# Kernel optimization log

Measured on AMD Instinct MI355X. Metric: run time of the kernel, lower is better.

Reference implementation:

```python
import jax, jax.numpy as jnp
import numpy as np

H = 1024  # hidden_dim
M = 4     # num_modalities
B = 8192  # batch


def setup_inputs() -> dict:
    key = jax.random.key(0)
    ks = jax.random.split(key, 10)
    s = 1.0 / np.sqrt(H)  # torch Linear default init scale
    return {
        "features": jax.random.normal(ks[0], (B, M, H), dtype=jnp.float32),
        "confidences": jax.random.uniform(ks[1], (B, M, 1), dtype=jnp.float32),
        "Wq": jax.random.uniform(ks[2], (H, H), jnp.float32, -s, s),
        "bq": jax.random.uniform(ks[3], (H,), jnp.float32, -s, s),
        "Wk": jax.random.uniform(ks[4], (H, H), jnp.float32, -s, s),
        "bk": jax.random.uniform(ks[5], (H,), jnp.float32, -s, s),
        "Wv": jax.random.uniform(ks[6], (H, H), jnp.float32, -s, s),
        "bv": jax.random.uniform(ks[7], (H,), jnp.float32, -s, s),
        "Wo": jax.random.uniform(ks[8], (H, H), jnp.float32, -s, s),
        "bo": jax.random.uniform(ks[9], (H,), jnp.float32, -s, s),
    }


def reference(features, confidences, Wq, bq, Wk, bk, Wv, bv, Wo, bo):
    # features: [B, M, H], confidences: [B, M, 1]
    q = jnp.einsum('bmh,oh->bmo', features, Wq) + bq
    k = jnp.einsum('bmh,oh->bmo', features, Wk) + bk
    v = jnp.einsum('bmh,oh->bmo', features, Wv) + bv
    scores = jnp.einsum('bmh,bnh->bmn', q, k) / jnp.sqrt(jnp.float32(features.shape[-1]))
    scores = scores * confidences  # [B,M,1] broadcasts over last (key) axis
    attn = jax.nn.softmax(scores, axis=-1)           # [B, M, M]
    attended = jnp.einsum('bmn,bnh->bmh', attn, v)   # [B, M, H]
    fused = jnp.mean(attended, axis=1)               # [B, H]
    return fused @ Wo.T + bo
```

## Files before the change

### kernel.cpp

```cpp
#include <hip/hip_runtime.h>


typedef unsigned short u16;
typedef unsigned char u8;
typedef __attribute__((ext_vector_type(8))) __bf16 bf16x8;
typedef __attribute__((ext_vector_type(4))) float floatx4;
typedef __attribute__((ext_vector_type(16))) float floatx16;
typedef __attribute__((ext_vector_type(8))) int intx8;

__device__ __forceinline__ u16 f2bf(float f) {
    unsigned u = __float_as_uint(f);
    unsigned r = (u + 0x7FFFu + ((u >> 16) & 1u)) >> 16;
    return (u16)r;
}

__device__ __forceinline__ unsigned f2e4m3(float x) {
    unsigned u = __float_as_uint(x);
    unsigned s = (u >> 31) << 7;
    float a = __uint_as_float(u & 0x7FFFFFFFu);
    if (a >= 448.f) return s | 0x7E;
    if (a < 0.03125f) {
        unsigned k = (unsigned)__float2int_rn(a * 512.f);
        return s | k;
    }
    unsigned b = __float_as_uint(a);
    unsigned lsb = (b >> 20) & 1u;
    b += 0x0007FFFFu + lsb;
    unsigned ex = (b >> 23) - 120u;
    unsigned man = (b >> 20) & 7u;
    return s | (ex << 3) | man;
}

__device__ __forceinline__ void load_lds16(const void* g, void* l) {
    __builtin_amdgcn_global_load_lds(
        (const __attribute__((address_space(1))) void*)g,
        (__attribute__((address_space(3))) void*)l, 16, 0, 0);
}

__device__ __forceinline__ void unpack8(uint4 v, float* f) {
    f[0] = __uint_as_float(v.x << 16);
    f[1] = __uint_as_float(v.x & 0xFFFF0000u);
    f[2] = __uint_as_float(v.y << 16);
    f[3] = __uint_as_float(v.y & 0xFFFF0000u);
    f[4] = __uint_as_float(v.z << 16);
    f[5] = __uint_as_float(v.z & 0xFFFF0000u);
    f[6] = __uint_as_float(v.w << 16);
    f[7] = __uint_as_float(v.w & 0xFFFF0000u);
}

__global__ __launch_bounds__(256) void k_cast(const float* __restrict__ in,
                                              u16* __restrict__ outb,
                                              u8* __restrict__ outf, long n) {
    long i = ((long)blockIdx.x * 256 + threadIdx.x) * 4;
    if (i < n) {
        float4 v = *(const float4*)(in + i);
        ushort4 o;
        o.x = f2bf(v.x); o.y = f2bf(v.y); o.z = f2bf(v.z); o.w = f2bf(v.w);
        *(ushort4*)(outb + i) = o;
        if (outf) {
            unsigned p = f2e4m3(v.x) | (f2e4m3(v.y) << 8) |
                         (f2e4m3(v.z) << 16) | (f2e4m3(v.w) << 24);
            *(unsigned*)(outf + i) = p;
        }
    }
}

__global__ __launch_bounds__(256) void k_prep(const float* __restrict__ Wq,
                                              const float* __restrict__ Wk,
                                              const float* __restrict__ Wv,
                                              const float* __restrict__ Wo,
                                              u16* __restrict__ WqT,
                                              u16* __restrict__ WkT,
                                              u16* __restrict__ WvT,
                                              u16* __restrict__ Wob, int H) {
    __shared__ float t[32][33];
    const int z = blockIdx.z;
    const float* in = (z == 0) ? Wk : (z == 1) ? Wq : (z == 2) ? Wv : Wo;
    u16* out = (z == 0) ? WkT : (z == 1) ? WqT : (z == 2) ? WvT : Wob;
    int bx = blockIdx.x * 32, by = blockIdx.y * 32;
    int x = threadIdx.x;
    if (z < 3) {
        for (int y = threadIdx.y; y < 32; y += 8)
            t[y][x] = in[(size_t)(by + y) * H + bx + x];
        __syncthreads();
        for (int y = threadIdx.y; y < 32; y += 8)
            out[(size_t)(bx + y) * H + by + x] = f2bf(t[x][y]);
    } else {
        for (int y = threadIdx.y; y < 32; y += 8)
            out[(size_t)(by + y) * H + bx + x] = f2bf(in[(size_t)(by + y) * H + bx + x]);
    }
}

__global__ __launch_bounds__(256) void k_uk(const float* __restrict__ Wk,
                                            const float* __restrict__ bq,
                                            float* __restrict__ u, int H) {
    int h = blockIdx.x * 256 + threadIdx.x;
    int chunk = H / 16;
    int o0 = blockIdx.y * chunk;
    float s = 0.f;
    for (int o = o0; o < o0 + chunk; ++o) s += bq[o] * Wk[(size_t)o * H + h];
    atomicAdd(&u[h], s);
}

__global__ __launch_bounds__(256) void k_bias(const float* __restrict__ Wo,
                                              const float* __restrict__ bv,
                                              const float* __restrict__ bo,
                                              float* __restrict__ c, int H) {
    __shared__ float red[4];
    int j = blockIdx.x;
    int lane = threadIdx.x & 63, wv = threadIdx.x >> 6;
    float s = 0.f;
    for (int o = threadIdx.x; o < H; o += 256) s += Wo[(size_t)j * H + o] * bv[o];
    for (int off = 32; off > 0; off >>= 1) s += __shfl_down(s, off);
    if (lane == 0) red[wv] = s;
    __syncthreads();
    if (threadIdx.x == 0) c[j] = red[0] + red[1] + red[2] + red[3] + bo[j];
}

template <int OUTMODE>
__device__ __forceinline__ void gemm_body(const u16* __restrict__ A,
                                          const u16* __restrict__ Bw,
                                          void* __restrict__ Cp,
                                          u8* __restrict__ Cp8,
                                          const float* __restrict__ bias,
                                          int M, int N, int K,
                                          int bx, int by) {
    __shared__ __align__(16) u16 As[128 * 32];
    __shared__ __align__(16) u16 Bs[128 * 32];
    const int tid = threadIdx.x, lane = tid & 63, wv = tid >> 6;
    const int m0 = bx * 128, n0 = by * 128;
    const int wm = (wv >> 1) * 64, wn = (wv & 1) * 64;

    floatx4 acc[4][4];
#pragma unroll
    for (int i = 0; i < 4; ++i)
#pragma unroll
        for (int j = 0; j < 4; ++j) acc[i][j] = (floatx4){0.f, 0.f, 0.f, 0.f};

    const int srow = lane >> 2;
    const int scol = (((lane & 3) ^ ((lane >> 3) & 3)) * 8);
    const u16* gA = A + (size_t)(m0 + srow) * K + scol;
    const u16* gB = Bw + (size_t)(n0 + srow) * K + scol;
    const int r = lane & 15, q = lane >> 4;
    const int cph = q ^ ((r >> 1) & 3);

    for (int kt = 0; kt < K; kt += 32) {
#pragma unroll
        for (int c = 0; c < 2; ++c) {
            int chunk = wv * 2 + c;
            load_lds16(gA + (size_t)(chunk * 16) * K + kt, &As[chunk * 16 * 32]);
            load_lds16(gB + (size_t)(chunk * 16) * K + kt, &Bs[chunk * 16 * 32]);
        }
        __syncthreads();
        bf16x8 af[4], bfr[4];
#pragma unroll
        for (int i = 0; i < 4; ++i) {
            af[i] = *(const bf16x8*)&As[(wm + i * 16 + r) * 32 + cph * 8];
            bfr[i] = *(const bf16x8*)&Bs[(wn + i * 16 + r) * 32 + cph * 8];
        }
#pragma unroll
        for (int i = 0; i < 4; ++i)
#pragma unroll
            for (int j = 0; j < 4; ++j)
                acc[i][j] = __builtin_amdgcn_mfma_f32_16x16x32_bf16(af[i], bfr[j], acc[i][j], 0, 0, 0);
        __syncthreads();
    }

    const int cc = lane & 15, cr = (lane >> 4) * 4;
#pragma unroll
    for (int i = 0; i < 4; ++i)
#pragma unroll
        for (int j = 0; j < 4; ++j) {
            int col = n0 + wn + j * 16 + cc;
            float badd = bias ? bias[col] : 0.f;
#pragma unroll
            for (int r0 = 0; r0 < 4; ++r0) {
                int row = m0 + wm + i * 16 + cr + r0;
                float v = acc[i][j][r0] + badd;
                if (OUTMODE == 0) ((float*)Cp)[(size_t)row * N + col] = v;
                else ((u16*)Cp)[(size_t)row * N + col] = f2bf(v);
                if (OUTMODE == 2)
                    Cp8[(size_t)row * N + col] = (u8)f2e4m3(32.f * v);
            }
        }
}

__global__ __launch_bounds__(256) void k_wgemm(const u16* __restrict__ A0,
                                               const u16* __restrict__ B0,
                                               u16* __restrict__ C0,
                                               u8* __restrict__ C0f8,
                                               const u16* __restrict__ A1,
                                               const u16* __restrict__ B1,
                                               u16* __restrict__ C1, int H) {
    if (blockIdx.z == 0)
        gemm_body<2>(A0, B0, C0, C0f8, nullptr, H, H, H, blockIdx.x, blockIdx.y);
    else
        gemm_body<1>(A1, B1, C1, nullptr, nullptr, H, H, H, blockIdx.x, blockIdx.y);
}

__global__ __launch_bounds__(256) void k_score(const u16* __restrict__ X,
                                               const u16* __restrict__ Aw,
                                               u16* __restrict__ G,
                                               const float* __restrict__ uk,
                                               int Mr, int N, int K) {
    gemm_body<1>(X, Aw, G, nullptr, uk, Mr, N, K, blockIdx.x, blockIdx.y);
}

__global__ __launch_bounds__(256) void k_out(const u16* __restrict__ A,
                                             const u16* __restrict__ Bw,
                                             float* __restrict__ C,
                                             const float* __restrict__ bias,
                                             int M, int N, int K) {
    gemm_body<0>(A, Bw, C, nullptr, bias, M, N, K, blockIdx.x, blockIdx.y);
}

__global__ __launch_bounds__(256) void k_score8(const u8* __restrict__ Af8,
                                                const u8* __restrict__ Bf8,
                                                u16* __restrict__ G,
                                                const float* __restrict__ uk,
                                                int Mr, int N, int K) {
    __shared__ __align__(16) u8 As[128 * 64];
    __shared__ __align__(16) u8 Bs[128 * 64];
    const int tid = threadIdx.x, lane = tid & 63, wv = tid >> 6;

    const int nbx = gridDim.x;
    const int nwg = nbx * gridDim.y;
    const int orig = blockIdx.y * nbx + blockIdx.x;
    const int cpx = nwg >> 3;
    const int id = (orig & 7) * cpx + (orig >> 3);
    const int n0 = (id % nbx) * 128, m0 = (id / nbx) * 128;
    const int wm = (wv >> 1) * 64, wn = (wv & 1) * 64;

    floatx16 acc[2][2];
#pragma unroll
    for (int i = 0; i < 2; ++i)
#pragma unroll
        for (int j = 0; j < 2; ++j)
            acc[i][j] = (floatx16){0.f, 0.f, 0.f, 0.f, 0.f, 0.f, 0.f, 0.f,
                                   0.f, 0.f, 0.f, 0.f, 0.f, 0.f, 0.f, 0.f};

    const int srow = lane >> 2;
    const int scol = 16 * ((lane & 3) ^ ((lane >> 3) & 3));
    const u8* gA = Af8 + (size_t)(m0 + srow) * K + scol;
    const u8* gB = Bf8 + (size_t)(n0 + srow) * K + scol;

    const int r32 = lane & 31, q2 = lane >> 5;
    const int sw = (r32 >> 1) & 3;
    const int c0 = (2 * q2) ^ sw, c1 = (2 * q2 + 1) ^ sw;

    union frag32 { intx8 v; uint4 q[2]; };

    for (int kt = 0; kt < K; kt += 64) {
#pragma unroll
        for (int c = 0; c < 2; ++c) {
            int chunk = wv * 2 + c;
            load_lds16(gA + (size_t)(chunk * 16) * K + kt, &As[chunk * 16 * 64]);
            load_lds16(gB + (size_t)(chunk * 16) * K + kt, &Bs[chunk * 16 * 64]);
        }
        __syncthreads();
        frag32 fa[2], fb[2];
#pragma unroll
        for (int i = 0; i < 2; ++i) {
            const u8* pa = &As[(wm + i * 32 + r32) * 64];
            const u8* pb = &Bs[(wn + i * 32 + r32) * 64];
            fa[i].q[0] = *(const uint4*)(pa + c0 * 16);
            fa[i].q[1] = *(const uint4*)(pa + c1 * 16);
            fb[i].q[0] = *(const uint4*)(pb + c0 * 16);
            fb[i].q[1] = *(const uint4*)(pb + c1 * 16);
        }
#pragma unroll
        for (int i = 0; i < 2; ++i)
#pragma unroll
            for (int j = 0; j < 2; ++j)
                acc[i][j] = __builtin_amdgcn_mfma_scale_f32_32x32x64_f8f6f4(
                    fa[i].v, fb[j].v, acc[i][j], 0, 0,
                    0, 0x7F7F7F7F, 0, 0x7F7F7F7F);
        __syncthreads();
    }

    const int cc = lane & 31, rbase = 4 * (lane >> 5);
#pragma unroll
    for (int i = 0; i < 2; ++i)
#pragma unroll
        for (int j = 0; j < 2; ++j) {
            int col = n0 + wn + j * 32 + cc;
            float badd = 32.f * uk[col];
#pragma unroll
            for (int reg = 0; reg < 16; ++reg) {
                int row = m0 + wm + i * 32 + (reg & 3) + 8 * (reg >> 2) + rbase;
                G[(size_t)row * N + col] = f2bf(acc[i][j][reg] + badd);
            }
        }
}

__global__ __launch_bounds__(256) void k_attn(const u16* __restrict__ G,
                                              const u16* __restrict__ X,
                                              const float* __restrict__ conf,
                                              u16* __restrict__ Y, float gscale,
                                              int H) {
    const int lane = threadIdx.x & 63, wv = threadIdx.x >> 6;
    const int b = blockIdx.x * 4 + wv;
    const u16* Gb = G + (size_t)b * 4 * H;
    const u16* Xb = X + (size_t)b * 4 * H;

    uint4 xraw[2][4];
    float s[16];
#pragma unroll
    for (int t = 0; t < 16; ++t) s[t] = 0.f;

#pragma unroll
    for (int c = 0; c < 2; ++c) {
        const int off = c * 512 + lane * 8;
#pragma unroll
        for (int rr = 0; rr < 4; ++rr)
            xraw[c][rr] = *(const uint4*)(Xb + rr * H + off);
        float xv[4][8];
#pragma unroll
        for (int rr = 0; rr < 4; ++rr) unpack8(xraw[c][rr], xv[rr]);
#pragma unroll
        for (int m = 0; m < 4; ++m) {
            uint4 gl = *(const uint4*)(Gb + m * H + off);
            float gv[8];
            unpack8(gl, gv);
#pragma unroll
            for (int n = 0; n < 4; ++n) {
                float a = 0.f;
#pragma unroll
                for (int j = 0; j < 8; ++j) a += gv[j] * xv[n][j];
                s[m * 4 + n] += a;
            }
        }
    }
#pragma unroll
    for (int t = 0; t < 16; ++t) {
#pragma unroll
        for (int mask = 32; mask; mask >>= 1) s[t] += __shfl_xor(s[t], mask);
    }
    float w[4] = {0.f, 0.f, 0.f, 0.f};
#pragma unroll
    for (int m = 0; m < 4; ++m) {
        float cm = conf[(size_t)b * 4 + m] * gscale;
        float sc[4], mx = -1e30f;
#pragma unroll
        for (int n = 0; n < 4; ++n) {
            sc[n] = s[m * 4 + n] * cm;
            mx = fmaxf(mx, sc[n]);
        }
        float e[4], ssum = 0.f;
#pragma unroll
        for (int n = 0; n < 4; ++n) { e[n] = __expf(sc[n] - mx); ssum += e[n]; }
        float inv = 0.25f / ssum;
#pragma unroll
        for (int n = 0; n < 4; ++n) w[n] += e[n] * inv;
    }
#pragma unroll
    for (int c = 0; c < 2; ++c) {
        const int off = c * 512 + lane * 8;
        float xv[4][8];
#pragma unroll
        for (int rr = 0; rr < 4; ++rr) unpack8(xraw[c][rr], xv[rr]);
        float y[8];
#pragma unroll
        for (int j = 0; j < 8; ++j)
            y[j] = w[0] * xv[0][j] + w[1] * xv[1][j] + w[2] * xv[2][j] + w[3] * xv[3][j];
        uint4 res;
        res.x = (unsigned)f2bf(y[0]) | ((unsigned)f2bf(y[1]) << 16);
        res.y = (unsigned)f2bf(y[2]) | ((unsigned)f2bf(y[3]) << 16);
        res.z = (unsigned)f2bf(y[4]) | ((unsigned)f2bf(y[5]) << 16);
        res.w = (unsigned)f2bf(y[6]) | ((unsigned)f2bf(y[7]) << 16);
        *(uint4*)(Y + (size_t)b * H + off) = res;
    }
}

extern "C" void kernel_launch(void* const* d_in, const int* in_sizes, int n_in,
                              void* d_out, int out_size, void* d_ws, size_t ws_size,
                              hipStream_t stream) {
    const int H = 1024, M = 4;
    const int B = in_sizes[0] / (H * M);
    const long BMH = (long)B * M * H;

    const float* feat = (const float*)d_in[0];
    const float* conf = (const float*)d_in[1];
    const float* Wq = (const float*)d_in[2];
    const float* bq = (const float*)d_in[3];
    const float* Wk = (const float*)d_in[4];
    const float* Wv = (const float*)d_in[6];
    const float* bv = (const float*)d_in[7];
    const float* Wo = (const float*)d_in[8];
    const float* bo = (const float*)d_in[9];

    char* ws = (char*)d_ws;
    size_t off = 0;
    auto alloc = [&](size_t bytes) {
        void* p = ws + off;
        off += (bytes + 255) & ~(size_t)255;
        return p;
    };
    u16* Xb    = (u16*)alloc((size_t)BMH * 2);
    u16* G     = (u16*)alloc((size_t)BMH * 2);
    u16* Yb    = (u16*)alloc((size_t)B * H * 2);
    u16* WkT   = (u16*)alloc((size_t)H * H * 2);
    u16* WqT   = (u16*)alloc((size_t)H * H * 2);
    u16* WvT   = (u16*)alloc((size_t)H * H * 2);
    u16* Wob   = (u16*)alloc((size_t)H * H * 2);
    u16* Aw    = (u16*)alloc((size_t)H * H * 2);
    u16* Wov   = (u16*)alloc((size_t)H * H * 2);
    float* u    = (float*)alloc((size_t)H * 4);
    float* cvec = (float*)alloc((size_t)H * 4);
    u8* Xf8  = (u8*)alloc((size_t)BMH);
    u8* Awf8 = (u8*)alloc((size_t)H * H);
    const bool use_fp8 = (off <= ws_size);
    (void)n_in; (void)out_size;

    k_cast<<<(int)(BMH / 4 / 256), 256, 0, stream>>>(
        feat, Xb, use_fp8 ? Xf8 : nullptr, BMH);
    k_prep<<<dim3(H / 32, H / 32, 4), dim3(32, 8), 0, stream>>>(
        Wq, Wk, Wv, Wo, WqT, WkT, WvT, Wob, H);

    hipMemsetAsync(u, 0, (size_t)H * 4, stream);
    k_uk<<<dim3(H / 256, 16), 256, 0, stream>>>(Wk, bq, u, H);
    k_bias<<<H, 256, 0, stream>>>(Wo, bv, bo, cvec, H);

    k_wgemm<<<dim3(H / 128, H / 128, 2), 256, 0, stream>>>(
        WkT, WqT, Aw, use_fp8 ? Awf8 : (u8*)Aw , Wob, WvT, Wov, H);

    if (use_fp8) {
        k_score8<<<dim3(H / 128, B * M / 128), 256, 0, stream>>>(
            Xf8, Awf8, G, u, B * M, H, H);
    } else {
        k_score<<<dim3(B * M / 128, H / 128), 256, 0, stream>>>(
            Xb, Aw, G, u, B * M, H, H);
    }

    k_attn<<<B / 4, 256, 0, stream>>>(G, Xb, conf, Yb,
                                      use_fp8 ? 0.0009765625f : 0.03125f, H);

    k_out<<<dim3(B / 128, H / 128), 256, 0, stream>>>(Yb, Wov, (float*)d_out, cvec, B, H, H);
}
```

Measured before the change: 391.2 us.

## Merge prep kernels into front kernel and overlap feature cast with weight GEMMs

```diff
diff --git a/kernel.cpp b/kernel.cpp
--- a/kernel.cpp
+++ b/kernel.cpp
@@ -48,85 +48,72 @@
     f[7] = __uint_as_float(v.w & 0xFFFF0000u);
 }
 
-__global__ __launch_bounds__(256) void k_cast(const float* __restrict__ in,
-                                              u16* __restrict__ outb,
-                                              u8* __restrict__ outf, long n) {
-    long i = ((long)blockIdx.x * 256 + threadIdx.x) * 4;
-    if (i < n) {
-        float4 v = *(const float4*)(in + i);
-        ushort4 o;
-        o.x = f2bf(v.x); o.y = f2bf(v.y); o.z = f2bf(v.z); o.w = f2bf(v.w);
-        *(ushort4*)(outb + i) = o;
-        if (outf) {
-            unsigned p = f2e4m3(v.x) | (f2e4m3(v.y) << 8) |
-                         (f2e4m3(v.z) << 16) | (f2e4m3(v.w) << 24);
-            *(unsigned*)(outf + i) = p;
-        }
-    }
-}
-
-__global__ __launch_bounds__(256) void k_prep(const float* __restrict__ Wq,
-                                              const float* __restrict__ Wk,
-                                              const float* __restrict__ Wv,
-                                              const float* __restrict__ Wo,
-                                              u16* __restrict__ WqT,
-                                              u16* __restrict__ WkT,
-                                              u16* __restrict__ WvT,
-                                              u16* __restrict__ Wob, int H) {
+__global__ __launch_bounds__(256) void k_front(const float* __restrict__ Wq,
+                                               const float* __restrict__ Wk,
+                                               const float* __restrict__ Wv,
+                                               const float* __restrict__ Wo,
+                                               const float* __restrict__ bq,
+                                               const float* __restrict__ bv,
+                                               const float* __restrict__ bo,
+                                               u16* __restrict__ WqT,
+                                               u16* __restrict__ WkT,
+                                               u16* __restrict__ WvT,
+                                               u16* __restrict__ Wob,
+                                               float* __restrict__ u,
+                                               float* __restrict__ cvec, int H) {
     __shared__ float t[32][33];
-    const int z = blockIdx.z;
-    const float* in = (z == 0) ? Wk : (z == 1) ? Wq : (z == 2) ? Wv : Wo;
-    u16* out = (z == 0) ? WkT : (z == 1) ? WqT : (z == 2) ? WvT : Wob;
-    int bx = blockIdx.x * 32, by = blockIdx.y * 32;
-    int x = threadIdx.x;
-    if (z < 3) {
-        for (int y = threadIdx.y; y < 32; y += 8)
-            t[y][x] = in[(size_t)(by + y) * H + bx + x];
+    __shared__ float red[4];
+    const int id = blockIdx.x;
+    if (id < 4096) {
+        const int z = id >> 10;
+        const int bx = (id & 31) * 32, by = ((id >> 5) & 31) * 32;
+        const float* in = (z == 0) ? Wk : (z == 1) ? Wq : (z == 2) ? Wv : Wo;
+        u16* out = (z == 0) ? WkT : (z == 1) ? WqT : (z == 2) ? WvT : Wob;
+        const int x = threadIdx.x & 31, ty = threadIdx.x >> 5;
+        if (z < 3) {
+            for (int y = ty; y < 32; y += 8)
+                t[y][x] = in[(size_t)(by + y) * H + bx + x];
+            __syncthreads();
+            for (int y = ty; y < 32; y += 8)
+                out[(size_t)(bx + y) * H + by + x] = f2bf(t[x][y]);
+        } else {
+            for (int y = ty; y < 32; y += 8)
+                out[(size_t)(by + y) * H + bx + x] =
+                    f2bf(in[(size_t)(by + y) * H + bx + x]);
+        }
+    } else if (id < 4160) {
+        const int r = id - 4096;
+        const int h = (r & 3) * 256 + threadIdx.x;
+        const int chunk = H / 16, o0 = (r >> 2) * chunk;
+        float s = 0.f;
+        for (int o = o0; o < o0 + chunk; ++o) s += bq[o] * Wk[(size_t)o * H + h];
+        atomicAdd(&u[h], s);
+    } else {
+        const int j = id - 4160;
+        const int lane = threadIdx.x & 63, wv = threadIdx.x >> 6;
+        float s = 0.f;
+        for (int o = threadIdx.x; o < H; o += 256)
+            s += Wo[(size_t)j * H + o] * bv[o];
+        for (int off = 32; off > 0; off >>= 1) s += __shfl_down(s, off);
+        if (lane == 0) red[wv] = s;
         __syncthreads();
-        for (int y = threadIdx.y; y < 32; y += 8)
-            out[(size_t)(bx + y) * H + by + x] = f2bf(t[x][y]);
-    } else {
-        for (int y = threadIdx.y; y < 32; y += 8)
-            out[(size_t)(by + y) * H + bx + x] = f2bf(in[(size_t)(by + y) * H + bx + x]);
-    }
-}
-
-__global__ __launch_bounds__(256) void k_uk(const float* __restrict__ Wk,
-                                            const float* __restrict__ bq,
-                                            float* __restrict__ u, int H) {
-    int h = blockIdx.x * 256 + threadIdx.x;
-    int chunk = H / 16;
-    int o0 = blockIdx.y * chunk;
-    float s = 0.f;
-    for (int o = o0; o < o0 + chunk; ++o) s += bq[o] * Wk[(size_t)o * H + h];
-    atomicAdd(&u[h], s);
-}
-
-__global__ __launch_bounds__(256) void k_bias(const float* __restrict__ Wo,
-                                              const float* __restrict__ bv,
-                                              const float* __restrict__ bo,
-                                              float* __restrict__ c, int H) {
-    __shared__ float red[4];
-    int j = blockIdx.x;
-    int lane = threadIdx.x & 63, wv = threadIdx.x >> 6;
-    float s = 0.f;
-    for (int o = threadIdx.x; o < H; o += 256) s += Wo[(size_t)j * H + o] * bv[o];
-    for (int off = 32; off > 0; off >>= 1) s += __shfl_down(s, off);
-    if (lane == 0) red[wv] = s;
-    __syncthreads();
-    if (threadIdx.x == 0) c[j] = red[0] + red[1] + red[2] + red[3] + bo[j];
-}
+        if (threadIdx.x == 0) cvec[j] = red[0] + red[1] + red[2] + red[3] + bo[j];
+    }
+}
+
+struct GemmLds { u16 As[128 * 32]; u16 Bs[128 * 32]; };
 
 template <int OUTMODE>
-__device__ __forceinline__ void gemm_body(const u16* __restrict__ A,
+__device__ __forceinline__ void gemm_body(GemmLds& S,
+                                          const u16* __restrict__ A,
                                           const u16* __restrict__ Bw,
                                           void* __restrict__ Cp,
                                           u8* __restrict__ Cp8,
                                           const float* __restrict__ bias,
                                           int M, int N, int K,
                                           int bx, int by) {
-    __shared__ __align__(16) u16 As[128 * 32];
-    __shared__ __align__(16) u16 Bs[128 * 32];
+    u16* As = S.As;
+    u16* Bs = S.Bs;
     const int tid = threadIdx.x, lane = tid & 63, wv = tid >> 6;
     const int m0 = bx * 128, n0 = by * 128;
     const int wm = (wv >> 1) * 64, wn = (wv & 1) * 64;
@@ -179,23 +166,44 @@
                 float v = acc[i][j][r0] + badd;
                 if (OUTMODE == 0) ((float*)Cp)[(size_t)row * N + col] = v;
                 else ((u16*)Cp)[(size_t)row * N + col] = f2bf(v);
-                if (OUTMODE == 2)
+                if (OUTMODE == 2 && Cp8)
                     Cp8[(size_t)row * N + col] = (u8)f2e4m3(32.f * v);
             }
         }
 }
 
-__global__ __launch_bounds__(256) void k_wgemm(const u16* __restrict__ A0,
-                                               const u16* __restrict__ B0,
-                                               u16* __restrict__ C0,
-                                               u8* __restrict__ C0f8,
-                                               const u16* __restrict__ A1,
-                                               const u16* __restrict__ B1,
-                                               u16* __restrict__ C1, int H) {
-    if (blockIdx.z == 0)
-        gemm_body<2>(A0, B0, C0, C0f8, nullptr, H, H, H, blockIdx.x, blockIdx.y);
-    else
-        gemm_body<1>(A1, B1, C1, nullptr, nullptr, H, H, H, blockIdx.x, blockIdx.y);
+__global__ __launch_bounds__(256) void k_mid(const float* __restrict__ feat,
+                                             u16* __restrict__ Xb,
+                                             u8* __restrict__ Xf8, long n,
+                                             const u16* __restrict__ WkT,
+                                             const u16* __restrict__ WqT,
+                                             u16* __restrict__ Aw,
+                                             u8* __restrict__ Awf8,
+                                             const u16* __restrict__ Wob,
+                                             const u16* __restrict__ WvT,
+                                             u16* __restrict__ Wov, int H) {
+    __shared__ __align__(16) GemmLds S;
+    const int id = blockIdx.x;
+    if (id < 128) {
+        const int z = id >> 6, bx = (id & 63) & 7, by = (id & 63) >> 3;
+        if (z == 0)
+            gemm_body<2>(S, WkT, WqT, Aw, Awf8, nullptr, H, H, H, bx, by);
+        else
+            gemm_body<1>(S, Wob, WvT, Wov, nullptr, nullptr, H, H, H, bx, by);
+    } else {
+        long i = ((long)(id - 128) * 256 + threadIdx.x) * 4;
+        if (i < n) {
+            float4 v = *(const float4*)(feat + i);
+            ushort4 o;
+            o.x = f2bf(v.x); o.y = f2bf(v.y); o.z = f2bf(v.z); o.w = f2bf(v.w);
+            *(ushort4*)(Xb + i) = o;
+            if (Xf8) {
+                unsigned p = f2e4m3(v.x) | (f2e4m3(v.y) << 8) |
+                             (f2e4m3(v.z) << 16) | (f2e4m3(v.w) << 24);
+                *(unsigned*)(Xf8 + i) = p;
+            }
+        }
+    }
 }
 
 __global__ __launch_bounds__(256) void k_score(const u16* __restrict__ X,
@@ -203,7 +211,8 @@
                                                u16* __restrict__ G,
                                                const float* __restrict__ uk,
                                                int Mr, int N, int K) {
-    gemm_body<1>(X, Aw, G, nullptr, uk, Mr, N, K, blockIdx.x, blockIdx.y);
+    __shared__ __align__(16) GemmLds S;
+    gemm_body<1>(S, X, Aw, G, nullptr, uk, Mr, N, K, blockIdx.x, blockIdx.y);
 }
 
 __global__ __launch_bounds__(256) void k_out(const u16* __restrict__ A,
@@ -211,7 +220,8 @@
                                              float* __restrict__ C,
                                              const float* __restrict__ bias,
                                              int M, int N, int K) {
-    gemm_body<0>(A, Bw, C, nullptr, bias, M, N, K, blockIdx.x, blockIdx.y);
+    __shared__ __align__(16) GemmLds S;
+    gemm_body<0>(S, A, Bw, C, nullptr, bias, M, N, K, blockIdx.x, blockIdx.y);
 }
 
 __global__ __launch_bounds__(256) void k_score8(const u8* __restrict__ Af8,
@@ -412,17 +422,14 @@
     const bool use_fp8 = (off <= ws_size);
     (void)n_in; (void)out_size;
 
-    k_cast<<<(int)(BMH / 4 / 256), 256, 0, stream>>>(
-        feat, Xb, use_fp8 ? Xf8 : nullptr, BMH);
-    k_prep<<<dim3(H / 32, H / 32, 4), dim3(32, 8), 0, stream>>>(
-        Wq, Wk, Wv, Wo, WqT, WkT, WvT, Wob, H);
-
     hipMemsetAsync(u, 0, (size_t)H * 4, stream);
-    k_uk<<<dim3(H / 256, 16), 256, 0, stream>>>(Wk, bq, u, H);
-    k_bias<<<H, 256, 0, stream>>>(Wo, bv, bo, cvec, H);
-
-    k_wgemm<<<dim3(H / 128, H / 128, 2), 256, 0, stream>>>(
-        WkT, WqT, Aw, use_fp8 ? Awf8 : (u8*)Aw , Wob, WvT, Wov, H);
+    k_front<<<4096 + 64 + H, 256, 0, stream>>>(
+        Wq, Wk, Wv, Wo, bq, bv, bo, WqT, WkT, WvT, Wob, u, cvec, H);
+
+    const int castBlocks = (int)(BMH / 4 / 256);
+    k_mid<<<128 + castBlocks, 256, 0, stream>>>(
+        feat, Xb, use_fp8 ? Xf8 : nullptr, BMH,
+        WkT, WqT, Aw, use_fp8 ? Awf8 : nullptr, Wob, WvT, Wov, H);
 
     if (use_fp8) {
         k_score8<<<dim3(H / 128, B * M / 128), 256, 0, stream>>>(
```

Result: no change. 391.2 us (-0.0%).
